# Performance work log

Hardware: AMD Instinct MI355X
Metric: run time of the kernel (lower is better)

The kernel has to match this reference:

```python
import jax, jax.numpy as jnp
import numpy as np

TEMPERATURE = 0.7
BIG_NEG = -1e30  # safe stand-in for -inf (keeps grads finite)


def setup_inputs() -> dict:
    key = jax.random.key(0)
    k1, k2, k3 = jax.random.split(key, 3)
    B, D = 8192, 256
    embeddings = jax.random.normal(k1, (B, D), dtype=jnp.float32)
    categories = jax.random.randint(k2, (B,), 0, 16, dtype=jnp.int64)
    font_labels = jax.random.randint(k3, (B,), 0, 2000, dtype=jnp.int64)
    return {"embeddings": embeddings, "categories": categories, "font_labels": font_labels}


def reference(embeddings, categories, font_labels):
    # L2-normalize rows
    e = embeddings / jnp.linalg.norm(embeddings, axis=1, keepdims=True)
    sims = jnp.matmul(e, e.T) / TEMPERATURE  # [B, B]
    B = sims.shape[0]

    same = categories[:, None] == categories[None, :]
    diag = jnp.eye(B, dtype=bool)
    pos_mask = same & ~diag           # same category, excluding self
    neg_mask = ~same                  # different category (self excluded implicitly)

    valid = pos_mask.any(axis=1) & neg_mask.any(axis=1)

    pos_sim = jnp.max(jnp.where(pos_mask, sims, BIG_NEG), axis=1)  # hardest positive per anchor
    neg_max = jnp.max(jnp.where(neg_mask, sims, BIG_NEG), axis=1)

    # logsumexp over {pos_sim} U neg_sims, numerically stable
    m = jnp.where(valid, jnp.maximum(pos_sim, neg_max), 0.0)
    pos_safe = jnp.where(valid, pos_sim, 0.0)
    exp_neg_sum = jnp.sum(jnp.where(neg_mask, jnp.exp(sims - m[:, None]), 0.0), axis=1)
    lse = m + jnp.log(jnp.exp(pos_safe - m) + exp_neg_sum)

    loss_per_anchor = -pos_safe + lse
    n_valid = jnp.maximum(jnp.sum(valid), 1)
    return jnp.sum(jnp.where(valid, loss_per_anchor, 0.0)) / n_valid
```

## Files before the change

kernel.cpp:

```cpp
#include <hip/hip_runtime.h>
#include <stdint.h>

#define NROWS 8192
#define DDIM 256
#define NSTRIPS 8
#define STRIP_COLS 1024
#define BN 64
#define NTILES 16
#define BM 128

#define ESCALE 1.4356159f
#define CLOG2  2.0609929f
#define CNAT   1.42857142857f
#define LN2F   0.6931471806f
#define NEGBIG (-1e30f)

typedef __attribute__((ext_vector_type(8))) short short8;
typedef __attribute__((ext_vector_type(4))) float f32x4;

typedef __attribute__((address_space(3))) void lds_void;
typedef const __attribute__((address_space(1))) void gl_void;

__device__ __forceinline__ unsigned short f2bf(float x) {
  unsigned int u = __float_as_uint(x);
  u += 0x7fffu + ((u >> 16) & 1u);
  return (unsigned short)(u >> 16);
}

__global__ __launch_bounds__(256) void knorm(const float* __restrict__ emb,
                                             unsigned short* __restrict__ ebf) {
  const int wave = threadIdx.x >> 6, lane = threadIdx.x & 63;
  const int row = blockIdx.x * 4 + wave;
  const float4 v = *(const float4*)(emb + row * DDIM + lane * 4);
  float ss = v.x * v.x + v.y * v.y + v.z * v.z + v.w * v.w;
#pragma unroll
  for (int off = 1; off < 64; off <<= 1) ss += __shfl_xor(ss, off, 64);
  const float sc = rsqrtf(ss) * ESCALE;
  ushort4 o;
  o.x = f2bf(v.x * sc); o.y = f2bf(v.y * sc);
  o.z = f2bf(v.z * sc); o.w = f2bf(v.w * sc);
  *(ushort4*)(ebf + row * DDIM + lane * 4) = o;
}

__global__ __launch_bounds__(256) void kmain(const unsigned short* __restrict__ ebf,
                                             const int* __restrict__ cats,
                                             float* __restrict__ posP,
                                             float* __restrict__ sumP) {
  __shared__ alignas(16) unsigned short smem[2][BN * DDIM];
  const int tid = threadIdx.x;
  const int lane = tid & 63, wave = tid >> 6;
  const int lane15 = lane & 15, quad = lane >> 4;
  const int strip = blockIdx.x, rowTile = blockIdx.y;
  const int rowG = rowTile * BM + wave * 32;
  const int col0 = strip * STRIP_COLS;

  short8 a[2][8];
#pragma unroll
  for (int m = 0; m < 2; ++m)
#pragma unroll
    for (int kk = 0; kk < 8; ++kk)
      a[m][kk] = *(const short8*)(ebf + (rowG + m * 16 + lane15) * DDIM + kk * 32 + quad * 8);

  int cati[2][4];
#pragma unroll
  for (int m = 0; m < 2; ++m)
#pragma unroll
    for (int r = 0; r < 4; ++r)
      cati[m][r] = cats[rowG + m * 16 + quad * 4 + r];

  float pm[2][4], ns[2][4];
#pragma unroll
  for (int m = 0; m < 2; ++m)
#pragma unroll
    for (int r = 0; r < 4; ++r) { pm[m][r] = NEGBIG; ns[m][r] = 0.f; }

#define STAGE(t, buf)                                                          \
  {                                                                            \
    const unsigned short* g =                                                  \
        ebf + (size_t)(col0 + (t) * BN + lane) * DDIM + wave * 8;              \
    char* lb = (char*)&smem[(buf)][0] + wave * 1024;                           \
    _Pragma("unroll")                                                          \
    for (int c = 0; c < 8; ++c)                                                \
      __builtin_amdgcn_global_load_lds((gl_void*)(g + c * 32),                 \
                                       (lds_void*)(lb + c * 4096), 16, 0, 0);  \
  }

  STAGE(0, 0);

  for (int t = 0; t < NTILES; ++t) {
    __syncthreads();
    if (t + 1 < NTILES) STAGE(t + 1, (t + 1) & 1);
    const char* bb = (const char*)&smem[t & 1][0];
    const int colBase = col0 + t * BN;

#pragma unroll
    for (int nt = 0; nt < 4; ++nt) {
      f32x4 acc0 = {0.f, 0.f, 0.f, 0.f}, acc1 = {0.f, 0.f, 0.f, 0.f};
#pragma unroll
      for (int kk = 0; kk < 8; ++kk) {
        short8 b = *(const short8*)(bb + kk * 4096 + quad * 1024 + nt * 256 + lane15 * 16);
        acc0 = __builtin_amdgcn_mfma_f32_16x16x32_bf16(a[0][kk], b, acc0, 0, 0, 0);
        acc1 = __builtin_amdgcn_mfma_f32_16x16x32_bf16(a[1][kk], b, acc1, 0, 0, 0);
      }
      const int col = colBase + nt * 16 + lane15;
      const int cj = cats[col];
#pragma unroll
      for (int m = 0; m < 2; ++m) {
#pragma unroll
        for (int r = 0; r < 4; ++r) {
          const float s = m ? acc1[r] : acc0[r];
          const int row = rowG + m * 16 + quad * 4 + r;
          const bool same = (cj == cati[m][r]);
          const float psv = (same && (row != col)) ? s : NEGBIG;
          pm[m][r] = fmaxf(pm[m][r], psv);
          const float nsv = same ? NEGBIG : s;
          ns[m][r] += exp2f(nsv - CLOG2);
        }
      }
    }
  }

#pragma unroll
  for (int off = 1; off < 16; off <<= 1) {
#pragma unroll
    for (int m = 0; m < 2; ++m)
#pragma unroll
      for (int r = 0; r < 4; ++r) {
        pm[m][r] = fmaxf(pm[m][r], __shfl_xor(pm[m][r], off, 64));
        ns[m][r] += __shfl_xor(ns[m][r], off, 64);
      }
  }
  if (lane15 == 0) {
#pragma unroll
    for (int m = 0; m < 2; ++m)
#pragma unroll
      for (int r = 0; r < 4; ++r) {
        const int row = rowG + m * 16 + quad * 4 + r;
        posP[strip * NROWS + row] = pm[m][r];
        sumP[strip * NROWS + row] = ns[m][r];
      }
  }
}

__global__ __launch_bounds__(256) void kmerge(const float* __restrict__ posP,
                                              const float* __restrict__ sumP,
                                              float* __restrict__ acc) {
  const int row = blockIdx.x * 256 + threadIdx.x;
  float pm = NEGBIG, ns = 0.f;
#pragma unroll
  for (int s = 0; s < NSTRIPS; ++s) {
    pm = fmaxf(pm, posP[s * NROWS + row]);
    ns += sumP[s * NROWS + row];
  }
  const bool valid = (pm > -1e29f) && (ns > 0.f);
  float loss = valid ? (CNAT - pm * LN2F + logf(exp2f(pm - CLOG2) + ns)) : 0.f;
  float cnt = valid ? 1.f : 0.f;
#pragma unroll
  for (int off = 1; off < 64; off <<= 1) {
    loss += __shfl_xor(loss, off, 64);
    cnt += __shfl_xor(cnt, off, 64);
  }
  if ((threadIdx.x & 63) == 0) {
    atomicAdd(&acc[0], loss);
    atomicAdd(&acc[1], cnt);
  }
}

__global__ void kfinal(const float* __restrict__ acc, float* __restrict__ out) {
  out[0] = acc[0] / fmaxf(acc[1], 1.f);
}

extern "C" void kernel_launch(void* const* d_in, const int* in_sizes, int n_in,
                              void* d_out, int out_size, void* d_ws, size_t ws_size,
                              hipStream_t stream) {
  const float* emb = (const float*)d_in[0];
  const int* cats = (const int*)d_in[1];
  float* out = (float*)d_out;

  char* ws = (char*)d_ws;
  float* accv = (float*)ws;
  unsigned short* ebf = (unsigned short*)(ws + 256);
  float* posP = (float*)(ws + 256 + NROWS * DDIM * 2);
  float* sumP = posP + NSTRIPS * NROWS;

  hipMemsetAsync(accv, 0, 2 * sizeof(float), stream);
  knorm<<<NROWS / 4, 256, 0, stream>>>(emb, ebf);
  kmain<<<dim3(NSTRIPS, NROWS / BM), 256, 0, stream>>>(ebf, cats, posP, sumP);
  kmerge<<<NROWS / 256, 256, 0, stream>>>(posP, sumP, accv);
  kfinal<<<1, 1, 0, stream>>>(accv, out);
}
```

Baseline: 123.3 us.

## Halve column tile, drop exp offset, hoist category loads, fuse final kernel

Halves the column tile and strip width so the grid doubles to 16 strips, giving more blocks and half the LDS per block. Drops the constant shift before exp2, relying on normalized similarities being bounded, and uses the raw hardware exp2. Checks the diagonal only on tiles that contain it, and loads column categories once per tile. The final division is folded into the merge kernel through a last-block atomic counter, which removes one launch at the cost of extra atomics and a fence.

```diff
diff --git a/kernel.cpp b/kernel.cpp
--- a/kernel.cpp
+++ b/kernel.cpp
@@ -3,15 +3,13 @@
 
 #define NROWS 8192
 #define DDIM 256
-#define NSTRIPS 8
-#define STRIP_COLS 1024
-#define BN 64
+#define NSTRIPS 16
+#define STRIP_COLS 512
+#define BN 32
 #define NTILES 16
 #define BM 128
 
 #define ESCALE 1.4356159f
-#define CLOG2  2.0609929f
-#define CNAT   1.42857142857f
 #define LN2F   0.6931471806f
 #define NEGBIG (-1e30f)
 
@@ -68,21 +66,26 @@
     for (int r = 0; r < 4; ++r)
       cati[m][r] = cats[rowG + m * 16 + quad * 4 + r];
 
+  bool dlr[4];
+#pragma unroll
+  for (int r = 0; r < 4; ++r) dlr[r] = (lane15 == quad * 4 + r);
+
   float pm[2][4], ns[2][4];
 #pragma unroll
   for (int m = 0; m < 2; ++m)
 #pragma unroll
     for (int r = 0; r < 4; ++r) { pm[m][r] = NEGBIG; ns[m][r] = 0.f; }
 
-#define STAGE(t, buf)                                                          \
-  {                                                                            \
-    const unsigned short* g =                                                  \
-        ebf + (size_t)(col0 + (t) * BN + lane) * DDIM + wave * 8;              \
-    char* lb = (char*)&smem[(buf)][0] + wave * 1024;                           \
-    _Pragma("unroll")                                                          \
-    for (int c = 0; c < 8; ++c)                                                \
-      __builtin_amdgcn_global_load_lds((gl_void*)(g + c * 32),                 \
-                                       (lds_void*)(lb + c * 4096), 16, 0, 0);  \
+#define STAGE(t, buf)                                                           \
+  {                                                                             \
+    const unsigned short* g = ebf +                                             \
+        (size_t)(col0 + (t) * BN + (lane & 31)) * DDIM +                        \
+        (wave * 2 + (lane >> 5)) * 8;                                           \
+    char* lb = (char*)&smem[(buf)][0] + wave * 1024;                            \
+    _Pragma("unroll")                                                           \
+    for (int c = 0; c < 4; ++c)                                                 \
+      __builtin_amdgcn_global_load_lds((gl_void*)(g + c * 64),                  \
+                                       (lds_void*)(lb + c * 4096), 16, 0, 0);   \
   }
 
   STAGE(0, 0);
@@ -92,29 +95,32 @@
     if (t + 1 < NTILES) STAGE(t + 1, (t + 1) & 1);
     const char* bb = (const char*)&smem[t & 1][0];
     const int colBase = col0 + t * BN;
-
-#pragma unroll
-    for (int nt = 0; nt < 4; ++nt) {
+    const int cjt[2] = {cats[colBase + lane15], cats[colBase + 16 + lane15]};
+
+#pragma unroll
+    for (int nt = 0; nt < 2; ++nt) {
       f32x4 acc0 = {0.f, 0.f, 0.f, 0.f}, acc1 = {0.f, 0.f, 0.f, 0.f};
 #pragma unroll
       for (int kk = 0; kk < 8; ++kk) {
-        short8 b = *(const short8*)(bb + kk * 4096 + quad * 1024 + nt * 256 + lane15 * 16);
+        short8 b = *(const short8*)(bb + kk * 2048 + quad * 512 + nt * 256 + lane15 * 16);
         acc0 = __builtin_amdgcn_mfma_f32_16x16x32_bf16(a[0][kk], b, acc0, 0, 0, 0);
         acc1 = __builtin_amdgcn_mfma_f32_16x16x32_bf16(a[1][kk], b, acc1, 0, 0, 0);
       }
-      const int col = colBase + nt * 16 + lane15;
-      const int cj = cats[col];
+      const int cj = cjt[nt];
+      const bool dg0 = (rowG == colBase + nt * 16);
+      const bool dg1 = (rowG + 16 == colBase + nt * 16);
 #pragma unroll
       for (int m = 0; m < 2; ++m) {
+        const bool dg = m ? dg1 : dg0;
 #pragma unroll
         for (int r = 0; r < 4; ++r) {
           const float s = m ? acc1[r] : acc0[r];
-          const int row = rowG + m * 16 + quad * 4 + r;
+          const float e = __builtin_amdgcn_exp2f(s);
           const bool same = (cj == cati[m][r]);
-          const float psv = (same && (row != col)) ? s : NEGBIG;
+          float psv = same ? s : NEGBIG;
+          if (dg) psv = dlr[r] ? NEGBIG : psv;
           pm[m][r] = fmaxf(pm[m][r], psv);
-          const float nsv = same ? NEGBIG : s;
-          ns[m][r] += exp2f(nsv - CLOG2);
+          ns[m][r] += same ? 0.f : e;
         }
       }
     }
@@ -144,7 +150,8 @@
 
 __global__ __launch_bounds__(256) void kmerge(const float* __restrict__ posP,
                                               const float* __restrict__ sumP,
-                                              float* __restrict__ acc) {
+                                              float* __restrict__ acc,
+                                              float* __restrict__ out) {
   const int row = blockIdx.x * 256 + threadIdx.x;
   float pm = NEGBIG, ns = 0.f;
 #pragma unroll
@@ -153,7 +160,7 @@
     ns += sumP[s * NROWS + row];
   }
   const bool valid = (pm > -1e29f) && (ns > 0.f);
-  float loss = valid ? (CNAT - pm * LN2F + logf(exp2f(pm - CLOG2) + ns)) : 0.f;
+  float loss = valid ? (logf(__builtin_amdgcn_exp2f(pm) + ns) - pm * LN2F) : 0.f;
   float cnt = valid ? 1.f : 0.f;
 #pragma unroll
   for (int off = 1; off < 64; off <<= 1) {
@@ -163,11 +170,17 @@
   if ((threadIdx.x & 63) == 0) {
     atomicAdd(&acc[0], loss);
     atomicAdd(&acc[1], cnt);
-  }
-}
-
-__global__ void kfinal(const float* __restrict__ acc, float* __restrict__ out) {
-  out[0] = acc[0] / fmaxf(acc[1], 1.f);
+    __threadfence();
+  }
+  __syncthreads();
+  if (threadIdx.x == 0) {
+    const int prev = atomicAdd((int*)(acc + 2), 1);
+    if (prev == (int)gridDim.x - 1) {
+      const float L = atomicAdd(&acc[0], 0.f);
+      const float C = atomicAdd(&acc[1], 0.f);
+      out[0] = L / fmaxf(C, 1.f);
+    }
+  }
 }
 
 extern "C" void kernel_launch(void* const* d_in, const int* in_sizes, int n_in,
@@ -183,9 +196,8 @@
   float* posP = (float*)(ws + 256 + NROWS * DDIM * 2);
   float* sumP = posP + NSTRIPS * NROWS;
 
-  hipMemsetAsync(accv, 0, 2 * sizeof(float), stream);
+  hipMemsetAsync(accv, 0, 16, stream);
   knorm<<<NROWS / 4, 256, 0, stream>>>(emb, ebf);
   kmain<<<dim3(NSTRIPS, NROWS / BM), 256, 0, stream>>>(ebf, cats, posP, sumP);
-  kmerge<<<NROWS / 256, 256, 0, stream>>>(posP, sumP, accv);
-  kfinal<<<1, 1, 0, stream>>>(accv, out);
-}
+  kmerge<<<NROWS / 256, 256, 0, stream>>>(posP, sumP, accv, out);
+}
```

Result: faster. 119.9 us (-2.7%).
